# Kernel optimization log

Measured on AMD Instinct MI355X. Metric: run time of the kernel, lower is better.

The kernel has to match this reference:

```python
import jax, jax.numpy as jnp
import numpy as np

CHI, CHO, K, PAD = 64, 64, 3, 1
EPS = 1e-5


def setup_inputs() -> dict:
    key = jax.random.key(0)
    ks = jax.random.split(key, 4)
    B, H, W = 4, 128, 128
    x = jax.random.normal(ks[0], (B, CHI, H, W), jnp.float32)
    # conv_offset: produces 3*dg*K*K = 27 channels (o1, o2, mask); init small so offsets are modest
    w_off = jax.random.normal(ks[1], (3 * K * K, CHI, K, K), jnp.float32) * 0.01
    b_off = jnp.zeros((3 * K * K,), jnp.float32)
    # main deformable conv weight/bias
    w = jax.random.normal(ks[2], (CHO, CHI, K, K), jnp.float32) * (1.0 / np.sqrt(CHI * K * K))
    b = jnp.zeros((CHO,), jnp.float32)
    # BatchNorm affine params
    gamma = jnp.ones((CHO,), jnp.float32)
    beta = jnp.zeros((CHO,), jnp.float32)
    return {"x": x, "w_off": w_off, "b_off": b_off, "w": w, "b": b, "gamma": gamma, "beta": beta}


def _deform_conv(x, w_off, b_off, w, b):
    B, C, H, W_ = x.shape
    # offset/mask prediction: plain 3x3 conv, pad 1 -> [B, 27, H, W]
    off = jax.lax.conv_general_dilated(
        x, w_off, (1, 1), ((PAD, PAD), (PAD, PAD)),
        dimension_numbers=("NCHW", "OIHW", "NCHW")) + b_off[None, :, None, None]
    o1, o2, m = jnp.split(off, 3, axis=1)
    # mmcv DCNv2: offset = cat(o1, o2) -> [B, 2*K*K, H, W], interleaved (dy, dx) per tap
    offset = jnp.concatenate([o1, o2], axis=1).reshape(B, K * K, 2, H, W_)
    mask = jax.nn.sigmoid(m)                      # [B, 9, H, W]
    dy, dx = offset[:, :, 0], offset[:, :, 1]     # [B, 9, H, W]

    ky, kx = jnp.meshgrid(jnp.arange(K), jnp.arange(K), indexing="ij")
    ky = ky.reshape(1, K * K, 1, 1).astype(x.dtype)
    kx = kx.reshape(1, K * K, 1, 1).astype(x.dtype)
    hh = jnp.arange(H, dtype=x.dtype).reshape(1, 1, H, 1)
    ww = jnp.arange(W_, dtype=x.dtype).reshape(1, 1, 1, W_)
    py = hh - PAD + ky + dy                       # sampling row coords [B,9,H,W]
    px = ww - PAD + kx + dx                       # sampling col coords [B,9,H,W]

    y0 = jnp.floor(py)
    x0 = jnp.floor(px)
    wy = py - y0
    wx = px - x0

    x_flat = x.reshape(B, C, H * W_)

    def gather(yi, xi):
        # bilinear corner gather with zero padding outside the feature map
        valid = ((yi >= 0) & (yi < H) & (xi >= 0) & (xi < W_)).astype(x.dtype)
        yc = jnp.clip(yi, 0, H - 1).astype(jnp.int32)
        xc = jnp.clip(xi, 0, W_ - 1).astype(jnp.int32)
        idx = (yc * W_ + xc).reshape(B, 1, -1)
        v = jnp.take_along_axis(x_flat, idx, axis=2).reshape(B, C, K * K, H, W_)
        return v * valid[:, None]

    v00 = gather(y0, x0)
    v01 = gather(y0, x0 + 1)
    v10 = gather(y0 + 1, x0)
    v11 = gather(y0 + 1, x0 + 1)

    wy_ = wy[:, None]
    wx_ = wx[:, None]
    val = (v00 * (1 - wy_) * (1 - wx_) + v01 * (1 - wy_) * wx_
           + v10 * wy_ * (1 - wx_) + v11 * wy_ * wx_)
    val = val * mask[:, None]                     # modulated sampling [B,C,9,H,W]

    out = jnp.einsum("bckhw,ock->bohw", val, w.reshape(CHO, CHI, K * K))
    return out + b[None, :, None, None]


def reference(x, w_off, b_off, w, b, gamma, beta):
    y = _deform_conv(x, w_off, b_off, w, b)
    # BatchNorm2d (training-mode forward: batch statistics, biased variance)
    mean = y.mean(axis=(0, 2, 3))
    var = y.var(axis=(0, 2, 3))
    yhat = (y - mean[None, :, None, None]) * jax.lax.rsqrt(var[None, :, None, None] + EPS)
    return jax.nn.relu(yhat * gamma[None, :, None, None] + beta[None, :, None, None])
```

## Files before the change

### kernel.cpp

```cpp
#include <hip/hip_runtime.h>
#include <math.h>

#define CHI 64
#define CHO 64
#define HH 128
#define WW 128
#define NB 4
#define KK 9
#define NOFF 27
#define EPSV 1e-5f
#define PLANE (HH * WW)
#define SP 72

typedef float f32x4 __attribute__((ext_vector_type(4)));
typedef short bf16x8 __attribute__((ext_vector_type(8)));
typedef unsigned int u32x4 __attribute__((ext_vector_type(4)));

__device__ __forceinline__ unsigned short f2bf(float f) {
    unsigned u = __float_as_uint(f);
    u += 0x7fff + ((u >> 16) & 1);
    return (unsigned short)(u >> 16);
}
__device__ __forceinline__ float bfl(unsigned u) { return __uint_as_float(u << 16); }
__device__ __forceinline__ float bfh(unsigned u) { return __uint_as_float(u & 0xffff0000u); }

__global__ __launch_bounds__(256) void prep_kernel(const float* __restrict__ x,
                                                   const float* __restrict__ w,
                                                   const float* __restrict__ w_off,
                                                   unsigned short* __restrict__ x_bf,
                                                   unsigned short* __restrict__ w_bf,
                                                   unsigned short* __restrict__ woA) {
    __shared__ unsigned short lt[128 * SP];
    if (blockIdx.x < 512) {
        const int id = blockIdx.x;
        const int b  = id >> 7;
        const int y  = id & 127;
        const int t  = threadIdx.x;
        const int ci = t >> 2, qx = t & 3;
        const float* src = x + ((size_t)(b * CHI + ci)) * PLANE + y * WW;
#pragma unroll
        for (int it = 0; it < 8; it++) {
            int xcol = (it * 4 + qx) * 4;
            float4 v = *(const float4*)(src + xcol);
            lt[(xcol + 0) * SP + ci] = f2bf(v.x);
            lt[(xcol + 1) * SP + ci] = f2bf(v.y);
            lt[(xcol + 2) * SP + ci] = f2bf(v.z);
            lt[(xcol + 3) * SP + ci] = f2bf(v.w);
        }
        __syncthreads();
        unsigned short* dst = x_bf + (size_t)id * (WW * 64);
#pragma unroll
        for (int it = 0; it < 4; it++) {
            int px  = it * 32 + (t >> 3);
            int ci8 = t & 7;
            u32x4 v = *(const u32x4*)&lt[px * SP + ci8 * 8];
            *(u32x4*)(dst + px * 64 + ci8 * 8) = v;
        }
    } else {
        int i = (blockIdx.x - 512) * 256 + threadIdx.x;
        {
            int j    = i & 7;
            int lane = (i >> 3) & 63;
            int ks   = (i >> 9) & 1;
            int ct   = (i >> 10) & 3;
            int kk   = i >> 12;
            int co   = ct * 16 + (lane & 15);
            int ci   = ks * 32 + ((lane >> 4) & 3) * 8 + j;
            w_bf[i]  = f2bf(w[(co * CHI + ci) * KK + kk]);
        }
        if (i < 18432) {
            int j    = i & 7;
            int lane = (i >> 3) & 63;
            int ct   = (i >> 9) & 1;
            int ks   = (i >> 10) & 1;
            int kk   = i >> 11;
            int c    = ct * 16 + (lane & 15);
            int ci   = ks * 32 + (lane >> 4) * 8 + j;
            woA[i]   = (c < NOFF) ? f2bf(w_off[(c * CHI + ci) * KK + kk]) : (unsigned short)0;
        }
    }
}

__global__ __launch_bounds__(256, 4) void deform_kernel(const unsigned short* __restrict__ x_bf,
                                                        const unsigned short* __restrict__ w_bf,
                                                        const unsigned short* __restrict__ woA,
                                                        const float* __restrict__ b_off,
                                                        float* __restrict__ out,
                                                        float* __restrict__ pstats) {
    const int id    = blockIdx.x;
    const int slot  = id & 7;
    const int b     = slot >> 1;
    const int rb    = id >> 3;
    const int h     = (slot & 1) * 64 + (rb >> 1);
    const int whalf = rb & 1;
    const int w0    = whalf * 64;
    const int tid   = threadIdx.x;
    const int lane  = tid & 63;
    const int wave  = __builtin_amdgcn_readfirstlane(tid >> 6);
    const int quad  = lane >> 4, pxin = lane & 15;
    const int pxl   = wave * 16 + pxin;

    __shared__ __align__(16) unsigned short xs[3 * 66 * SP];
    __shared__ float offs[64 * 27];
    __shared__ float red[512];

    const unsigned short* xb = x_bf + (size_t)b * (PLANE * 64);
#pragma unroll
    for (int ky = 0; ky < 3; ky++) {
        int hr = h - 1 + ky;
        for (int base = tid; base < 528; base += 256) {
            int col = base >> 3, ci8 = base & 7;
            int wc  = w0 - 1 + col;
            bool ok = ((unsigned)hr < HH) && ((unsigned)wc < WW);
            u32x4 v = {0u, 0u, 0u, 0u};
            if (ok) v = *(const u32x4*)(xb + ((size_t)(hr * WW + wc)) * 64 + ci8 * 8);
            *(u32x4*)&xs[(ky * 66 + col) * SP + ci8 * 8] = v;
        }
    }
    __syncthreads();

    f32x4 oacc0 = {0.f, 0.f, 0.f, 0.f};
    f32x4 oacc1 = {0.f, 0.f, 0.f, 0.f};
#pragma unroll 3
    for (int kk = 0; kk < KK; kk++) {
        const int ky = kk / 3, kx = kk - ky * 3;
#pragma unroll
        for (int ks = 0; ks < 2; ks++) {
            const bf16x8* wa = (const bf16x8*)woA + (size_t)((kk * 2 + ks) * 2) * 64;
            bf16x8 A0 = wa[lane];
            bf16x8 A1 = wa[64 + lane];
            bf16x8 B = *(const bf16x8*)&xs[(ky * 66 + wave * 16 + pxin + kx) * SP
                                           + ks * 32 + quad * 8];
            oacc0 = __builtin_amdgcn_mfma_f32_16x16x32_bf16(A0, B, oacc0, 0, 0, 0);
            oacc1 = __builtin_amdgcn_mfma_f32_16x16x32_bf16(A1, B, oacc1, 0, 0, 0);
        }
    }

#pragma unroll
    for (int r = 0; r < 4; r++) {
        int c0 = quad * 4 + r;
        offs[pxl * 27 + c0] = oacc0[r];
        int c1 = 16 + quad * 4 + r;
        if (c1 < NOFF) offs[pxl * 27 + c1] = oacc1[r];
    }
    __syncthreads();

    f32x4 acc[4];
#pragma unroll
    for (int t = 0; t < 4; t++) acc[t] = (f32x4){0.f, 0.f, 0.f, 0.f};

    const int wpix = w0 + wave * 16 + pxin;
    const unsigned short* xbq = xb + quad * 8;

#pragma unroll 3
    for (int kk = 0; kk < KK; kk++) {
        const int ky = kk / 3, kx = kk - ky * 3;
        float dyv = offs[pxl * 27 + 2 * kk]     + b_off[2 * kk];
        float dxv = offs[pxl * 27 + 2 * kk + 1] + b_off[2 * kk + 1];
        float mov = offs[pxl * 27 + 18 + kk]    + b_off[18 + kk];

        float m   = 1.f / (1.f + __expf(-mov));
        float py  = (float)(h - 1 + ky) + dyv;
        float px_ = (float)(wpix - 1 + kx) + dxv;
        float fy0 = floorf(py), fx0 = floorf(px_);
        float wy = py - fy0, wx = px_ - fx0;
        int y0 = (int)fy0, x0 = (int)fx0;
        int y1 = y0 + 1, x1 = x0 + 1;
        bool vy0 = (unsigned)y0 < HH, vy1 = (unsigned)y1 < HH;
        bool vx0 = (unsigned)x0 < WW, vx1 = (unsigned)x1 < WW;
        float a00 = (vy0 && vx0) ? (1.f - wy) * (1.f - wx) * m : 0.f;
        float a01 = (vy0 && vx1) ? (1.f - wy) * wx * m : 0.f;
        float a10 = (vy1 && vx0) ? wy * (1.f - wx) * m : 0.f;
        float a11 = (vy1 && vx1) ? wy * wx * m : 0.f;
        int cy0 = min(max(y0, 0), HH - 1), cy1 = min(max(y1, 0), HH - 1);
        int cx0 = min(max(x0, 0), WW - 1), cx1 = min(max(x1, 0), WW - 1);
        const unsigned o00 = ((unsigned)(cy0 * WW + cx0)) << 6;
        const unsigned o01 = ((unsigned)(cy0 * WW + cx1)) << 6;
        const unsigned o10 = ((unsigned)(cy1 * WW + cx0)) << 6;
        const unsigned o11 = ((unsigned)(cy1 * WW + cx1)) << 6;

        u32x4 g00a = *(const u32x4*)(xbq + o00);
        u32x4 g01a = *(const u32x4*)(xbq + o01);
        u32x4 g10a = *(const u32x4*)(xbq + o10);
        u32x4 g11a = *(const u32x4*)(xbq + o11);
        u32x4 g00b = *(const u32x4*)(xbq + o00 + 32);
        u32x4 g01b = *(const u32x4*)(xbq + o01 + 32);
        u32x4 g10b = *(const u32x4*)(xbq + o10 + 32);
        u32x4 g11b = *(const u32x4*)(xbq + o11 + 32);

        const bf16x8* wb = (const bf16x8*)w_bf + (size_t)(kk * 8) * 64;
        bf16x8 A[8];
#pragma unroll
        for (int q = 0; q < 8; q++) A[q] = wb[q * 64 + lane];

        bf16x8 B0, B1;
#pragma unroll
        for (int d = 0; d < 4; d++) {
            float tl = a00 * bfl(g00a[d]) + a01 * bfl(g01a[d])
                     + a10 * bfl(g10a[d]) + a11 * bfl(g11a[d]);
            float th = a00 * bfh(g00a[d]) + a01 * bfh(g01a[d])
                     + a10 * bfh(g10a[d]) + a11 * bfh(g11a[d]);
            B0[2 * d]     = (short)f2bf(tl);
            B0[2 * d + 1] = (short)f2bf(th);
            float ul = a00 * bfl(g00b[d]) + a01 * bfl(g01b[d])
                     + a10 * bfl(g10b[d]) + a11 * bfl(g11b[d]);
            float uh = a00 * bfh(g00b[d]) + a01 * bfh(g01b[d])
                     + a10 * bfh(g10b[d]) + a11 * bfh(g11b[d]);
            B1[2 * d]     = (short)f2bf(ul);
            B1[2 * d + 1] = (short)f2bf(uh);
        }

#pragma unroll
        for (int t = 0; t < 4; t++) {
            acc[t] = __builtin_amdgcn_mfma_f32_16x16x32_bf16(A[t * 2 + 0], B0, acc[t], 0, 0, 0);
            acc[t] = __builtin_amdgcn_mfma_f32_16x16x32_bf16(A[t * 2 + 1], B1, acc[t], 0, 0, 0);
        }
    }

#pragma unroll
    for (int t = 0; t < 4; t++) {
#pragma unroll
        for (int r = 0; r < 4; r++) {
            int co = t * 16 + quad * 4 + r;
            out[(((size_t)b * CHO + co) * HH + h) * WW + w0 + wave * 16 + pxin] =
                acc[t][r];
        }
    }

#pragma unroll
    for (int t = 0; t < 4; t++) {
#pragma unroll
        for (int r = 0; r < 4; r++) {
            float s  = acc[t][r];
            float s2 = s * s;
#pragma unroll
            for (int mk = 1; mk < 16; mk <<= 1) {
                s  += __shfl_xor(s, mk, 64);
                s2 += __shfl_xor(s2, mk, 64);
            }
            if (pxin == 0) {
                int co = t * 16 + quad * 4 + r;
                red[(0 * 4 + wave) * 64 + co] = s;
                red[(1 * 4 + wave) * 64 + co] = s2;
            }
        }
    }
    __syncthreads();
    if (tid < 128) {
        int part = tid >> 6, idx = tid & 63;
        float v = red[(part * 4 + 0) * 64 + idx] + red[(part * 4 + 1) * 64 + idx]
                + red[(part * 4 + 2) * 64 + idx] + red[(part * 4 + 3) * 64 + idx];
        pstats[(size_t)(part * 64 + idx) * 1024 + id] = v;
    }
}

__global__ __launch_bounds__(256) void statsbn_kernel(float* __restrict__ y,
                                                      const float* __restrict__ pstats,
                                                      const float* __restrict__ bias,
                                                      const float* __restrict__ gamma,
                                                      const float* __restrict__ beta) {
    const int co  = blockIdx.x & 63;
    const int seg = blockIdx.x >> 6;
    const int t   = threadIdx.x;

    const float* ps  = pstats + (size_t)co * 1024;
    const float* ps2 = pstats + (size_t)(64 + co) * 1024;
    float s  = ps[t]  + ps[t + 256]  + ps[t + 512]  + ps[t + 768];
    float s2 = ps2[t] + ps2[t + 256] + ps2[t + 512] + ps2[t + 768];
#pragma unroll
    for (int o = 32; o > 0; o >>= 1) {
        s  += __shfl_down(s, o, 64);
        s2 += __shfl_down(s2, o, 64);
    }
    __shared__ float ls[8];
    int lane = t & 63, wv = t >> 6;
    if (lane == 0) { ls[wv] = s; ls[4 + wv] = s2; }
    __syncthreads();
    float S0 = ls[0] + ls[1] + ls[2] + ls[3];
    float S2 = ls[4] + ls[5] + ls[6] + ls[7];
    float bi = bias[co];
    float Sb  = S0 + 65536.f * bi;
    float S2b = S2 + 2.f * bi * S0 + 65536.f * bi * bi;
    const float inv_n = 1.f / 65536.f;
    float mean = Sb * inv_n;
    float var  = S2b * inv_n - mean * mean;
    float sc = gamma[co] * rsqrtf(var + EPSV);
    float sh = beta[co] - mean * sc + bi * sc;

    const int b = seg >> 1, half = seg & 1;
    float4* p = (float4*)(y + ((size_t)(b * CHO + co)) * PLANE + half * 8192);
#pragma unroll
    for (int it = 0; it < 8; it++) {
        float4 v = p[it * 256 + t];
        v.x = fmaxf(fmaf(v.x, sc, sh), 0.f);
        v.y = fmaxf(fmaf(v.y, sc, sh), 0.f);
        v.z = fmaxf(fmaf(v.z, sc, sh), 0.f);
        v.w = fmaxf(fmaf(v.w, sc, sh), 0.f);
        p[it * 256 + t] = v;
    }
}

extern "C" void kernel_launch(void* const* d_in, const int* in_sizes, int n_in,
                              void* d_out, int out_size, void* d_ws, size_t ws_size,
                              hipStream_t stream) {
    const float* x     = (const float*)d_in[0];
    const float* w_off = (const float*)d_in[1];
    const float* b_off = (const float*)d_in[2];
    const float* wmat  = (const float*)d_in[3];
    const float* bvec  = (const float*)d_in[4];
    const float* gamma = (const float*)d_in[5];
    const float* beta  = (const float*)d_in[6];
    float* out = (float*)d_out;

    char* ws = (char*)d_ws;
    unsigned short* w_bf  = (unsigned short*)(ws + 1024);
    unsigned short* woA   = (unsigned short*)(ws + 74752);
    unsigned short* x_bf  = (unsigned short*)(ws + 139264);
    float* pstats         = (float*)(ws + 8527872);

    prep_kernel<<<656, 256, 0, stream>>>(x, wmat, w_off, x_bf, w_bf, woA);
    deform_kernel<<<1024, 256, 0, stream>>>(x_bf, w_bf, woA, b_off, out, pstats);
    statsbn_kernel<<<512, 256, 0, stream>>>(out, pstats, bvec, gamma, beta);
}
```

Measured before the change: 138.1 us.

## Split output channels across two blocks and drop shared-memory input staging

```diff
diff --git a/kernel.cpp b/kernel.cpp
--- a/kernel.cpp
+++ b/kernel.cpp
@@ -81,59 +81,58 @@
     }
 }
 
-__global__ __launch_bounds__(256, 4) void deform_kernel(const unsigned short* __restrict__ x_bf,
+__global__ __launch_bounds__(256, 8) void deform_kernel(const unsigned short* __restrict__ x_bf,
                                                         const unsigned short* __restrict__ w_bf,
                                                         const unsigned short* __restrict__ woA,
                                                         const float* __restrict__ b_off,
                                                         float* __restrict__ out,
                                                         float* __restrict__ pstats) {
-    const int id    = blockIdx.x;
-    const int slot  = id & 7;
-    const int b     = slot >> 1;
-    const int rb    = id >> 3;
-    const int h     = (slot & 1) * 64 + (rb >> 1);
-    const int whalf = rb & 1;
-    const int w0    = whalf * 64;
-    const int tid   = threadIdx.x;
-    const int lane  = tid & 63;
-    const int wave  = __builtin_amdgcn_readfirstlane(tid >> 6);
-    const int quad  = lane >> 4, pxin = lane & 15;
-    const int pxl   = wave * 16 + pxin;
-
-    __shared__ __align__(16) unsigned short xs[3 * 66 * SP];
+    const int id     = blockIdx.x;
+    const int slot   = id & 7;
+    const int b      = slot >> 1;
+    const int cohalf = (id >> 3) & 1;
+    const int rb     = id >> 4;
+    const int h      = (slot & 1) * 64 + (rb >> 1);
+    const int whalf  = rb & 1;
+    const int w0     = whalf * 64;
+    const int pg     = slot + 8 * rb;
+    const int tid    = threadIdx.x;
+    const int lane   = tid & 63;
+    const int wave   = __builtin_amdgcn_readfirstlane(tid >> 6);
+    const int quad   = lane >> 4, pxin = lane & 15;
+    const int pxl    = wave * 16 + pxin;
+    const int wpix   = w0 + pxl;
+
     __shared__ float offs[64 * 27];
-    __shared__ float red[512];
-
-    const unsigned short* xb = x_bf + (size_t)b * (PLANE * 64);
-#pragma unroll
-    for (int ky = 0; ky < 3; ky++) {
-        int hr = h - 1 + ky;
-        for (int base = tid; base < 528; base += 256) {
-            int col = base >> 3, ci8 = base & 7;
-            int wc  = w0 - 1 + col;
-            bool ok = ((unsigned)hr < HH) && ((unsigned)wc < WW);
-            u32x4 v = {0u, 0u, 0u, 0u};
-            if (ok) v = *(const u32x4*)(xb + ((size_t)(hr * WW + wc)) * 64 + ci8 * 8);
-            *(u32x4*)&xs[(ky * 66 + col) * SP + ci8 * 8] = v;
-        }
-    }
-    __syncthreads();
+    __shared__ float red[2 * 4 * 32];
+
+    const unsigned short* xb  = x_bf + (size_t)b * (PLANE * 64);
+    const unsigned short* xbq = xb + quad * 8;
 
     f32x4 oacc0 = {0.f, 0.f, 0.f, 0.f};
     f32x4 oacc1 = {0.f, 0.f, 0.f, 0.f};
 #pragma unroll 3
     for (int kk = 0; kk < KK; kk++) {
         const int ky = kk / 3, kx = kk - ky * 3;
-#pragma unroll
-        for (int ks = 0; ks < 2; ks++) {
-            const bf16x8* wa = (const bf16x8*)woA + (size_t)((kk * 2 + ks) * 2) * 64;
-            bf16x8 A0 = wa[lane];
-            bf16x8 A1 = wa[64 + lane];
-            bf16x8 B = *(const bf16x8*)&xs[(ky * 66 + wave * 16 + pxin + kx) * SP
-                                           + ks * 32 + quad * 8];
-            oacc0 = __builtin_amdgcn_mfma_f32_16x16x32_bf16(A0, B, oacc0, 0, 0, 0);
-            oacc1 = __builtin_amdgcn_mfma_f32_16x16x32_bf16(A1, B, oacc1, 0, 0, 0);
-        }
+        const int hr = h - 1 + ky;
+        const int wc = wpix - 1 + kx;
+        const bool ok = ((unsigned)hr < HH) && ((unsigned)wc < WW);
+        const unsigned po = ok ? ((unsigned)(hr * WW + wc)) << 6 : 0u;
+        bf16x8 Bv0 = {0, 0, 0, 0, 0, 0, 0, 0};
+        bf16x8 Bv1 = {0, 0, 0, 0, 0, 0, 0, 0};
+        if (ok) {
+            Bv0 = *(const bf16x8*)(xbq + po);
+            Bv1 = *(const bf16x8*)(xbq + po + 32);
+        }
+        const bf16x8* wa = (const bf16x8*)woA + (size_t)(kk * 4) * 64;
+        bf16x8 A0k0 = wa[lane];
+        bf16x8 A1k0 = wa[64 + lane];
+        bf16x8 A0k1 = wa[128 + lane];
+        bf16x8 A1k1 = wa[192 + lane];
+        oacc0 = __builtin_amdgcn_mfma_f32_16x16x32_bf16(A0k0, Bv0, oacc0, 0, 0, 0);
+        oacc1 = __builtin_amdgcn_mfma_f32_16x16x32_bf16(A1k0, Bv0, oacc1, 0, 0, 0);
+        oacc0 = __builtin_amdgcn_mfma_f32_16x16x32_bf16(A0k1, Bv1, oacc0, 0, 0, 0);
+        oacc1 = __builtin_amdgcn_mfma_f32_16x16x32_bf16(A1k1, Bv1, oacc1, 0, 0, 0);
     }
 
 #pragma unroll
@@ -145,12 +144,9 @@
     }
     __syncthreads();
 
-    f32x4 acc[4];
-#pragma unroll
-    for (int t = 0; t < 4; t++) acc[t] = (f32x4){0.f, 0.f, 0.f, 0.f};
-
-    const int wpix = w0 + wave * 16 + pxin;
-    const unsigned short* xbq = xb + quad * 8;
+    f32x4 acc[2];
+    acc[0] = (f32x4){0.f, 0.f, 0.f, 0.f};
+    acc[1] = (f32x4){0.f, 0.f, 0.f, 0.f};
 
 #pragma unroll 3
     for (int kk = 0; kk < KK; kk++) {
@@ -189,9 +185,10 @@
         u32x4 g11b = *(const u32x4*)(xbq + o11 + 32);
 
         const bf16x8* wb = (const bf16x8*)w_bf + (size_t)(kk * 8) * 64;
-        bf16x8 A[8];
-#pragma unroll
-        for (int q = 0; q < 8; q++) A[q] = wb[q * 64 + lane];
+        bf16x8 A00 = wb[((2 * cohalf + 0) * 2 + 0) * 64 + lane];
+        bf16x8 A01 = wb[((2 * cohalf + 0) * 2 + 1) * 64 + lane];
+        bf16x8 A10 = wb[((2 * cohalf + 1) * 2 + 0) * 64 + lane];
+        bf16x8 A11 = wb[((2 * cohalf + 1) * 2 + 1) * 64 + lane];
 
         bf16x8 B0, B1;
 #pragma unroll
@@ -210,25 +207,23 @@
             B1[2 * d + 1] = (short)f2bf(uh);
         }
 
-#pragma unroll
-        for (int t = 0; t < 4; t++) {
-            acc[t] = __builtin_amdgcn_mfma_f32_16x16x32_bf16(A[t * 2 + 0], B0, acc[t], 0, 0, 0);
-            acc[t] = __builtin_amdgcn_mfma_f32_16x16x32_bf16(A[t * 2 + 1], B1, acc[t], 0, 0, 0);
-        }
-    }
-
-#pragma unroll
-    for (int t = 0; t < 4; t++) {
+        acc[0] = __builtin_amdgcn_mfma_f32_16x16x32_bf16(A00, B0, acc[0], 0, 0, 0);
+        acc[0] = __builtin_amdgcn_mfma_f32_16x16x32_bf16(A01, B1, acc[0], 0, 0, 0);
+        acc[1] = __builtin_amdgcn_mfma_f32_16x16x32_bf16(A10, B0, acc[1], 0, 0, 0);
+        acc[1] = __builtin_amdgcn_mfma_f32_16x16x32_bf16(A11, B1, acc[1], 0, 0, 0);
+    }
+
+#pragma unroll
+    for (int t = 0; t < 2; t++) {
 #pragma unroll
         for (int r = 0; r < 4; r++) {
-            int co = t * 16 + quad * 4 + r;
-            out[(((size_t)b * CHO + co) * HH + h) * WW + w0 + wave * 16 + pxin] =
-                acc[t][r];
-        }
-    }
-
-#pragma unroll
-    for (int t = 0; t < 4; t++) {
+            int co = (2 * cohalf + t) * 16 + quad * 4 + r;
+            out[(((size_t)b * CHO + co) * HH + h) * WW + wpix] = acc[t][r];
+        }
+    }
+
+#pragma unroll
+    for (int t = 0; t < 2; t++) {
 #pragma unroll
         for (int r = 0; r < 4; r++) {
             float s  = acc[t][r];
@@ -239,18 +234,18 @@
                 s2 += __shfl_xor(s2, mk, 64);
             }
             if (pxin == 0) {
-                int co = t * 16 + quad * 4 + r;
-                red[(0 * 4 + wave) * 64 + co] = s;
-                red[(1 * 4 + wave) * 64 + co] = s2;
+                int cl = t * 16 + quad * 4 + r;
+                red[(0 * 4 + wave) * 32 + cl] = s;
+                red[(1 * 4 + wave) * 32 + cl] = s2;
             }
         }
     }
     __syncthreads();
-    if (tid < 128) {
-        int part = tid >> 6, idx = tid & 63;
-        float v = red[(part * 4 + 0) * 64 + idx] + red[(part * 4 + 1) * 64 + idx]
-                + red[(part * 4 + 2) * 64 + idx] + red[(part * 4 + 3) * 64 + idx];
-        pstats[(size_t)(part * 64 + idx) * 1024 + id] = v;
+    if (tid < 64) {
+        int part = tid >> 5, idx = tid & 31;
+        float v = red[(part * 4 + 0) * 32 + idx] + red[(part * 4 + 1) * 32 + idx]
+                + red[(part * 4 + 2) * 32 + idx] + red[(part * 4 + 3) * 32 + idx];
+        pstats[(size_t)(part * 64 + cohalf * 32 + idx) * 1024 + pg] = v;
     }
 }
 
@@ -319,6 +314,6 @@
     float* pstats         = (float*)(ws + 8527872);
 
     prep_kernel<<<656, 256, 0, stream>>>(x, wmat, w_off, x_bf, w_bf, woA);
-    deform_kernel<<<1024, 256, 0, stream>>>(x_bf, w_bf, woA, b_off, out, pstats);
+    deform_kernel<<<2048, 256, 0, stream>>>(x_bf, w_bf, woA, b_off, out, pstats);
     statsbn_kernel<<<512, 256, 0, stream>>>(out, pstats, bvec, gamma, beta);
 }
```

Result: slower. 258.5 us (+87.2%).
